# Kernel tuning notes

Hardware: AMD Instinct MI355X
Metric: run time of the kernel (lower is better)

## Reference

```python
import jax, jax.numpy as jnp
import numpy as np

BS, GS, E, KMAX = 128, 2000, 128, 4
CLIP = 10.0
NEG = -1e30


def _gru(x, hprev, Wih, Whh, bih, bhh):
    # torch.nn.GRUCell math
    gi = x @ Wih.T + bih
    gh = hprev @ Whh.T + bhh
    ir, iz, i_n = jnp.split(gi, 3, axis=-1)
    hr, hz, h_n = jnp.split(gh, 3, axis=-1)
    r = jax.nn.sigmoid(ir + hr)
    z = jax.nn.sigmoid(iz + hz)
    n = jnp.tanh(i_n + r * h_n)
    return (1.0 - z) * n + z * hprev


def setup_inputs() -> dict:
    key = jax.random.key(0)
    it = iter(jax.random.split(key, 40))
    s = 1.0 / float(np.sqrt(E))
    u = lambda shape: jax.random.uniform(next(it), shape, jnp.float32, -s, s)
    inp = {
        "h": jax.random.normal(next(it), (BS, GS, E), jnp.float32),
        "rec": jax.random.randint(next(it), (BS, GS), 0, GS, dtype=jnp.int32),
        "context2": jax.random.normal(next(it), (BS, 9), jnp.float32),
        "visited_time": jax.random.randint(next(it), (BS, GS), 0, GS, dtype=jnp.int32),
        "last_action": jax.random.randint(next(it), (BS, 1), 0, GS, dtype=jnp.int32),
        "fixed_action": jax.random.randint(next(it), (BS, KMAX), 0, GS, dtype=jnp.int32),
    }
    for n in ["W_K1", "W_K2", "W_K3", "W_K4", "W_Q1", "W_Q2", "W_Q3", "W_Q4", "W_init"]:
        inp[n] = u((E, E))
    for n in ["b_init", "V1", "V2", "init_query"]:
        inp[n] = u((E,))
    for r in ["rnn1", "rnn2"]:
        inp[r + "_Wih"] = u((3 * E, E))
        inp[r + "_Whh"] = u((3 * E, E))
        inp[r + "_bih"] = u((3 * E,))
        inp[r + "_bhh"] = u((3 * E,))
    return inp


def _forward(h, rec, visited_time, last_action, fixed_action,
             W_K1, W_K2, W_K3, W_K4, W_Q1, W_Q2, W_Q3, W_Q4, V1, V2,
             W_init, b_init, init_query,
             rnn1_Wih, rnn1_Whh, rnn1_bih, rnn1_bhh,
             rnn2_Wih, rnn2_Whh, rnn2_bih, rnn2_bhh):
    bs, gs, e = h.shape
    cols = jnp.arange(gs)[None, :]          # [1, gs]
    rows = jnp.arange(bs)
    # K projections of h are loop-invariant: hoist them (same math as in-loop recompute)
    K1h = jnp.einsum('bge,fe->bgf', h, W_K1)
    K2h = jnp.einsum('bge,fe->bgf', h, W_K2)
    K3h = jnp.einsum('bge,fe->bgf', h, W_K3)
    K4h = jnp.einsum('bge,fe->bgf', h, W_K4)
    q1 = q2 = h.mean(1) @ W_init.T + b_init
    input_q1 = input_q2 = jnp.broadcast_to(init_query, (bs, e))
    mask = jnp.zeros((bs, gs), bool)
    stopped = jnp.ones((bs,), bool)
    nol = jnp.full((bs, 1), -1, jnp.int32)   # next_of_last_action
    ai = jnp.zeros((bs, KMAX), jnp.int32)    # action_index
    kl = jnp.zeros((bs, KMAX + 1), jnp.int32)
    kr = jnp.zeros((bs, KMAX), jnp.int32)
    ll = jnp.zeros((bs,), h.dtype)
    vtt = None
    for i in range(KMAX):
        q1 = _gru(input_q1, q1, rnn1_Wih, rnn1_Whh, rnn1_bih, rnn1_bhh)
        q2 = _gru(input_q2, q2, rnn2_Wih, rnn2_Whh, rnn2_bih, rnn2_bhh)
        s1 = (V1 * jnp.tanh(K1h + (q1 @ W_Q1.T)[:, None, :] + K3h * (q1 @ W_Q3.T)[:, None, :])).sum(-1)
        s2 = (V2 * jnp.tanh(K2h + (q2 @ W_Q2.T)[:, None, :] + K4h * (q2 @ W_Q4.T)[:, None, :])).sum(-1)
        logits = jnp.tanh(s1 + s2) * CLIP
        logits = jnp.where(mask, NEG, logits)
        if i == 0:
            logits = jnp.where(cols == last_action, NEG, logits)
        action = fixed_action[:, i:i + 1]
        if i > 0:
            action = jnp.where(stopped[:, None], ai[:, 0:1], action)
        logp = jax.nn.log_softmax(logits, axis=-1)
        loss_now = jnp.take_along_axis(logp, action, 1)[:, 0]
        ll = ll + (loss_now if i == 0 else jnp.where(stopped, 0.0, loss_now))
        nna = jnp.take_along_axis(rec, action, 1)  # next_of_new_action [bs,1]
        ai = ai.at[:, i].set(action[:, 0])
        kl = kl.at[:, i].set(jnp.where(stopped, action[:, 0], kl[:, i]))
        kr = kr.at[:, (i - 1) % KMAX].set(jnp.where(stopped, kr[:, (i - 1) % KMAX], action[:, 0]))
        kl = kl.at[:, i + 1].set(nna[:, 0])
        input_q1 = h[rows, action[:, 0]]
        input_q2 = jnp.where(stopped[:, None], input_q1, h[rows, nol[:, 0] % gs])
        eq = (action == nol)[:, 0]
        stopped = eq if i == 0 else (stopped | eq)
        kl = kl.at[:, i].set(jnp.where(stopped, kl[:, (i - 1) % (KMAX + 1)], kl[:, i]))
        kr = kr.at[:, i].set(jnp.where(stopped, kr[:, (i - 1) % KMAX], kr[:, i]))
        if i == 0:
            vtt = (visited_time - jnp.take_along_axis(visited_time, action, 1)) % gs
        vtt_a = jnp.take_along_axis(vtt, action, 1)
        mask = vtt <= vtt_a
        if i == 0:
            mask = mask | (vtt > gs - 2)
        mask = jnp.where(stopped[:, None] & (cols == action), False, mask)
        allow = (~stopped) & (nna[:, 0] == ai[:, 0])
        mask = jnp.where(allow[:, None] & (cols == ai[:, 0:1]), False, mask)
        nol = jnp.where(stopped[:, None], jnp.int32(-1), nna)
    kr = kr.at[:, KMAX - 1].set(jnp.where(~stopped, kl[:, KMAX], kr[:, KMAX - 1]))
    action_all = jnp.concatenate([ai, kl[:, :KMAX], kr], axis=-1)  # [bs, 3*KMAX]
    return action_all, ll


def reference(h, rec, context2, visited_time, last_action, fixed_action,
              W_K1, W_K2, W_K3, W_K4, W_Q1, W_Q2, W_Q3, W_Q4,
              V1, V2, W_init, b_init, init_query,
              rnn1_Wih, rnn1_Whh, rnn1_bih, rnn1_bhh,
              rnn2_Wih, rnn2_Whh, rnn2_bih, rnn2_bhh):
    # context2 unused: with_explore_stat_feature=False path (learned V1/V2)
    return _forward(h, rec, visited_time, last_action, fixed_action,
                    W_K1, W_K2, W_K3, W_K4, W_Q1, W_Q2, W_Q3, W_Q4, V1, V2,
                    W_init, b_init, init_query,
                    rnn1_Wih, rnn1_Whh, rnn1_bih, rnn1_bhh,
                    rnn2_Wih, rnn2_Whh, rnn2_bih, rnn2_bhh)
```

## Files before the change

### kernel.cpp

```cpp
#include <hip/hip_runtime.h>
#include <math.h>

#define BS 128
#define GS 2000
#define E  128
#define KMAXI 4
#define CLIPV 10.0f
#define NEGV  -1.0e30f

typedef __bf16 bf16_t;
typedef __bf16 bf16x8 __attribute__((ext_vector_type(8)));
typedef float fx4 __attribute__((ext_vector_type(4)));
typedef float fx2 __attribute__((ext_vector_type(2)));

__device__ __forceinline__ float fast_sigmoid(float x){ return 1.0f/(1.0f+__expf(-x)); }
__device__ __forceinline__ float fast_tanhf(float x){
    float e = __expf(2.0f*x);
    return 1.0f - 2.0f/(e + 1.0f);
}
__device__ __forceinline__ float pade_tanh(float x){
    float t = __builtin_amdgcn_fmed3f(x, -3.0f, 3.0f);
    float r = t*t;
    float num = t*(27.0f + r);
    float den = fmaf(9.0f, r, 27.0f);
    return num * __builtin_amdgcn_rcpf(den);
}
__device__ __forceinline__ fx2 tanh2_poly(fx2 x){
    fx2 t;
    t.x = __builtin_amdgcn_fmed3f(x.x, -3.0f, 3.0f);
    t.y = __builtin_amdgcn_fmed3f(x.y, -3.0f, 3.0f);
    fx2 r = t*t;
    fx2 q = r*(-0.0015650f) + 0.03172875f;
    q = q*r + (-0.23082094f);
    q = q*r + 0.979947f;
    return t*q;
}
__device__ __forceinline__ int pymod_s(int a){ return a < 0 ? a + GS : a; }

__device__ __forceinline__ void load_lds16(const bf16_t* g, bf16_t* l){
    __builtin_amdgcn_global_load_lds(
        (const __attribute__((address_space(1))) void*)g,
        (__attribute__((address_space(3))) void*)l, 16, 0, 0);
}

#define SC_STRIDE 64

__global__ __launch_bounds__(256) void k_hmean(
    const float* __restrict__ h, float* __restrict__ hpart,
    const int* __restrict__ rec, const int* __restrict__ vtime,
    const int* __restrict__ last_action, const int* __restrict__ fixed_action,
    int* __restrict__ sc, float* __restrict__ out)
{
    int b = blockIdx.x, p = blockIdx.y, tid = threadIdx.x;
    if (p == 16){
        if (b != 0) return;
        int t = tid;
        if (t >= BS) return;
        int stopped = 1, nol = -1;
        int ai[4]={0,0,0,0}, kl[5]={0,0,0,0,0}, kr[4]={0,0,0,0};
        int a0 = 0;
        int* scb = sc + t*SC_STRIDE;
        for (int it=0; it<KMAXI; ++it){
            int action = (it==0) ? fixed_action[t*KMAXI]
                                 : (stopped ? ai[0] : fixed_action[t*KMAXI+it]);
            int old_stopped = stopped;
            if (it==0) a0 = action;
            int vta = (it==0) ? 0 : pymod_s(vtime[(size_t)t*GS+action] - vtime[(size_t)t*GS+a0]);
            int nna = rec[(size_t)t*GS+action];
            int eq  = (action == nol) ? 1 : 0;
            int new_stopped = (it==0) ? eq : (stopped | eq);
            int ai0 = (it==0) ? action : ai[0];
            int allow = (!new_stopped) && (nna == ai0);

            ai[it] = action;
            if (old_stopped)  kl[it] = action;
            if (!old_stopped) kr[(it+3)&3] = action;
            kl[it+1] = nna;
            if (new_stopped) kl[it] = kl[(it+4)%5];
            if (new_stopped) kr[it] = kr[(it+3)&3];

            int row1 = action;
            int i2 = pymod_s(nol);
            int row2 = old_stopped ? row1 : i2;

            int* s_it = scb + 8 + it*8;
            s_it[0]=action; s_it[1]=old_stopped; s_it[2]=new_stopped;
            s_it[3]=allow;  s_it[4]=vta; s_it[5]=row1; s_it[6]=row2;

            nol = new_stopped ? -1 : nna;
            stopped = new_stopped;
        }
        scb[0] = a0;
        if (!stopped) kr[3] = kl[4];
        out[BS*12 + t] = 0.0f;
        for (int j=0;j<4;++j) out[t*12+j]   = (float)ai[j];
        for (int j=0;j<4;++j) out[t*12+4+j] = (float)kl[j];
        for (int j=0;j<4;++j) out[t*12+8+j] = (float)kr[j];
        return;
    }
    int e4 = (tid & 31) * 4;
    int gsub = tid >> 5;
    float4 acc = {0.f,0.f,0.f,0.f};
    int g0 = p*125, g1 = g0+125;
    for (int g = g0 + gsub; g < g1; g += 8){
        float4 v = *(const float4*)(h + ((size_t)b*GS + g)*E + e4);
        acc.x += v.x; acc.y += v.y; acc.z += v.z; acc.w += v.w;
    }
    __shared__ float ps[8][E];
    *(float4*)(&ps[gsub][e4]) = acc;
    __syncthreads();
    if (tid < E){
        float s = 0.f;
        #pragma unroll
        for (int j=0;j<8;++j) s += ps[j][tid];
        hpart[(b*16+p)*E + tid] = s;
    }
}

__device__ __forceinline__ float dot32(const float* a, const float* __restrict__ w){
    const float4* a4=(const float4*)a; const float4* w4=(const float4*)w;
    float s=0.f;
    #pragma unroll 8
    for (int i=0;i<32;++i){ float4 x=a4[i], y=w4[i]; s += x.x*y.x + x.y*y.y + x.z*y.z + x.w*y.w; }
    return s;
}

__global__ __launch_bounds__(384) void k_gru4(
    const float* __restrict__ hpart, const float* __restrict__ W_init,
    const float* __restrict__ b_init, const float* __restrict__ init_query,
    const float* __restrict__ h, const int* __restrict__ sc,
    const float* __restrict__ Wih1, const float* __restrict__ Whh1,
    const float* __restrict__ bih1, const float* __restrict__ bhh1,
    const float* __restrict__ Wih2, const float* __restrict__ Whh2,
    const float* __restrict__ bih2, const float* __restrict__ bhh2,
    const float* __restrict__ WQ1, const float* __restrict__ WQ2,
    const float* __restrict__ WQ3, const float* __restrict__ WQ4,
    const float* __restrict__ WK1, const float* __restrict__ WK2,
    const float* __restrict__ WK3, const float* __restrict__ WK4,
    float* __restrict__ add_buf, bf16_t* __restrict__ Mb)
{
    int b = blockIdx.x, rnn = blockIdx.y, t = threadIdx.x;
    const float* Wih = rnn ? Wih2 : Wih1;
    const float* Whh = rnn ? Whh2 : Whh1;
    const float* bih = rnn ? bih2 : bih1;
    const float* bhh = rnn ? bhh2 : bhh1;
    const float* WQa = rnn ? WQ2 : WQ1;
    const float* WQm = rnn ? WQ4 : WQ3;
    const float* WKa = rnn ? WK2 : WK1;
    const float* WKm = rnn ? WK4 : WK3;

    __shared__ float xv[E], hv[E], mv[E];
    __shared__ float gi_s[3*E], gh_s[3*E];

    if (t < E){
        float s = 0.f;
        for (int p=0;p<16;++p) s += hpart[(b*16+p)*E + t];
        xv[t] = s * (1.0f/(float)GS);
    }
    __syncthreads();
    if (t < E) hv[t] = b_init[t] + dot32(xv, W_init + (size_t)t*E);
    __syncthreads();
    if (t < E) xv[t] = init_query[t];
    __syncthreads();

    for (int s=0; s<KMAXI; ++s){
        if (s>0){
            if (t < E){
                int row = sc[b*SC_STRIDE + 8 + (s-1)*8 + (rnn==0 ? 5 : 6)];
                xv[t] = h[((size_t)b*GS + row)*E + t];
            }
            __syncthreads();
        }
        {
            float gi = bih[t] + dot32(xv, Wih + (size_t)t*E);
            float gh = bhh[t] + dot32(hv, Whh + (size_t)t*E);
            gi_s[t] = gi; gh_s[t] = gh;
        }
        __syncthreads();
        if (t < E){
            float r = fast_sigmoid(gi_s[t]     + gh_s[t]);
            float z = fast_sigmoid(gi_s[t+E]   + gh_s[t+E]);
            float n = fast_tanhf  (gi_s[t+2*E] + r*gh_s[t+2*E]);
            hv[t] = (1.f-z)*n + z*hv[t];
        }
        __syncthreads();
        int slot = s*2 + rnn;
        if (t < 2*E){
            int r = t & (E-1);
            const float* W = (t < E) ? WQa : WQm;
            float v = dot32(hv, W + (size_t)r*E);
            if (t < E) add_buf[(size_t)slot*BS*E + b*E + r] = v;
            else       mv[r] = v;
        }
        __syncthreads();
        {
            bf16x8* outp = (bf16x8*)(Mb + ((size_t)slot*BS + b)*E*E);
            for (int u = t; u < 2048; u += 384){
                int f = u >> 4, e8 = u & 15;
                int e0 = e8*8;
                float mf = mv[f];
                float4 a0 = *(const float4*)(WKa + (size_t)f*E + e0);
                float4 a1 = *(const float4*)(WKa + (size_t)f*E + e0 + 4);
                float4 m0 = *(const float4*)(WKm + (size_t)f*E + e0);
                float4 m1 = *(const float4*)(WKm + (size_t)f*E + e0 + 4);
                bf16x8 o;
                o[0]=(bf16_t)(a0.x + m0.x*mf);
                o[1]=(bf16_t)(a0.y + m0.y*mf);
                o[2]=(bf16_t)(a0.z + m0.z*mf);
                o[3]=(bf16_t)(a0.w + m0.w*mf);
                o[4]=(bf16_t)(a1.x + m1.x*mf);
                o[5]=(bf16_t)(a1.y + m1.y*mf);
                o[6]=(bf16_t)(a1.z + m1.z*mf);
                o[7]=(bf16_t)(a1.w + m1.w*mf);
                outp[f*16 + (e8 ^ (f&7))] = o;
            }
        }
        __syncthreads();
    }
}

__global__ __launch_bounds__(256,2) void k_scores(
    const float* __restrict__ hf, const bf16_t* __restrict__ Mb,
    const float* __restrict__ add_buf,
    const float* __restrict__ V1, const float* __restrict__ V2,
    float* __restrict__ raw4)
{
    __shared__ bf16_t sM[2][E*E];
    int b = blockIdx.x, yc = blockIdx.y, tid = threadIdx.x;
    int wave = tid >> 6, lane = tid & 63;
    int qd = lane >> 4, cl = lane & 15;
    int gbase = yc*128 + wave*32;

    float vv_r[2][8];
    #pragma unroll
    for (int tf=0; tf<8; ++tf){
        vv_r[0][tf] = V1[tf*16+cl];
        vv_r[1][tf] = V2[tf*16+cl];
    }

    bf16x8 afr[2][4];
    #pragma unroll
    for (int set=0; set<2; ++set){
        int grow = gbase + set*16 + cl;
        if (grow >= GS) grow = GS-1;
        const float* hrow = hf + ((size_t)b*GS + grow)*E;
        #pragma unroll
        for (int s=0;s<4;++s){
            const float* p = hrow + s*32 + qd*8;
            float4 u0 = *(const float4*)(p);
            float4 u1 = *(const float4*)(p+4);
            bf16x8 a;
            a[0]=(bf16_t)u0.x; a[1]=(bf16_t)u0.y; a[2]=(bf16_t)u0.z; a[3]=(bf16_t)u0.w;
            a[4]=(bf16_t)u1.x; a[5]=(bf16_t)u1.y; a[6]=(bf16_t)u1.z; a[7]=(bf16_t)u1.w;
            afr[set][s]=a;
        }
    }

    for (int it=0; it<KMAXI; ++it){
        fx2 s00={0.f,0.f}, s01={0.f,0.f}, s10={0.f,0.f}, s11={0.f,0.f};

        const bf16_t* G0 = Mb + ((size_t)(it*2+0)*BS + b)*E*E;
        const bf16_t* G1 = Mb + ((size_t)(it*2+1)*BS + b)*E*E;
        float av_r[2][8];
        #pragma unroll
        for (int tf=0; tf<8; ++tf){
            av_r[0][tf] = add_buf[(size_t)(it*2+0)*BS*E + b*E + tf*16+cl];
            av_r[1][tf] = add_buf[(size_t)(it*2+1)*BS*E + b*E + tf*16+cl];
        }

        __syncthreads();
        #pragma unroll
        for (int j=0;j<8;++j){
            int c = wave*512 + j*64 + lane;
            load_lds16(G0 + (size_t)c*8, &sM[0][0] + (size_t)c*8);
            load_lds16(G1 + (size_t)c*8, &sM[1][0] + (size_t)c*8);
        }
        __syncthreads();

        #pragma unroll
        for (int arm=0; arm<2; ++arm){
            const bf16_t* sMc = &sM[arm][0];
            #pragma unroll
            for (int tf=0; tf<8; ++tf){
                int f = tf*16 + cl;
                bf16x8 b1[4];
                #pragma unroll
                for (int s=0;s<4;++s){
                    int e8 = s*4 + qd;
                    b1[s] = *(const bf16x8*)(sMc + ((size_t)(f*16 + (e8 ^ (f&7))))*8);
                }
                float av = av_r[arm][tf];
                fx4 a0 = {av,av,av,av};
                fx4 a1 = {av,av,av,av};
                #pragma unroll
                for (int s=0;s<4;++s){
                    a0 = __builtin_amdgcn_mfma_f32_16x16x32_bf16(afr[0][s], b1[s], a0, 0,0,0);
                    a1 = __builtin_amdgcn_mfma_f32_16x16x32_bf16(afr[1][s], b1[s], a1, 0,0,0);
                }
                fx2 vv2 = {vv_r[arm][tf], vv_r[arm][tf]};
                s00 += vv2 * tanh2_poly((fx2){a0[0], a0[1]});
                s01 += vv2 * tanh2_poly((fx2){a0[2], a0[3]});
                s10 += vv2 * tanh2_poly((fx2){a1[0], a1[1]});
                s11 += vv2 * tanh2_poly((fx2){a1[2], a1[3]});
            }
        }

        #pragma unroll
        for (int set=0;set<2;++set){
            fx2 pa = set ? s10 : s00;
            fx2 pb = set ? s11 : s01;
            float v[4] = {pa.x, pa.y, pb.x, pb.y};
            #pragma unroll
            for (int r=0;r<4;++r){
                float s = v[r];
                s += __shfl_xor(s, 1); s += __shfl_xor(s, 2);
                s += __shfl_xor(s, 4); s += __shfl_xor(s, 8);
                v[r] = s;
            }
            if (cl==0){
                int gi = gbase + set*16 + qd*4;
                if (gi+3 < GS){
                    float4 o;
                    o.x = CLIPV*pade_tanh(v[0]);
                    o.y = CLIPV*pade_tanh(v[1]);
                    o.z = CLIPV*pade_tanh(v[2]);
                    o.w = CLIPV*pade_tanh(v[3]);
                    *(float4*)(raw4 + ((size_t)it*BS + b)*GS + gi) = o;
                }
            }
        }
    }
}

__global__ __launch_bounds__(256) void k_ll(
    const float* __restrict__ raw4, const int* __restrict__ sc,
    const int* __restrict__ vtime, const int* __restrict__ last_action,
    float* __restrict__ out)
{
    __shared__ float sL[GS];
    __shared__ float red[256];
    int b = blockIdx.x, it = blockIdx.y, t = threadIdx.x;
    const int* scb = sc + b*SC_STRIDE;
    const int* s_it = scb + 8 + it*8;
    int action = s_it[0], olds = s_it[1];
    if (it>0 && olds) return;
    int a0 = scb[0];
    int la = last_action[b];
    int vt0 = vtime[(size_t)b*GS + a0];
    int ap=0, nsp=0, alp=0, vtp=0, p = it-1;
    if (it>0){
        const int* s_p = scb + 8 + p*8;
        ap = s_p[0]; nsp = s_p[2]; alp = s_p[3]; vtp = s_p[4];
    }
    for (int g=t; g<GS; g+=256){
        float l = raw4[((size_t)it*BS + b)*GS + g];
        int m;
        if (it==0){
            m = (g==la);
        } else {
            int d = vtime[(size_t)b*GS+g] - vt0;
            if (d < 0) d += GS;
            m = (d <= vtp) ? 1 : 0;
            if (p==0 && d > GS-2) m = 1;
            if (nsp && g==ap)     m = 0;
            if (alp && g==a0)     m = 0;
        }
        sL[g] = m ? NEGV : l;
    }
    __syncthreads();
    float mx = -3.0e38f;
    for (int g=t; g<GS; g+=256) mx = fmaxf(mx, sL[g]);
    red[t]=mx; __syncthreads();
    for (int s=128;s>0;s>>=1){ if(t<s) red[t]=fmaxf(red[t],red[t+s]); __syncthreads(); }
    mx = red[0]; __syncthreads();
    float sm = 0.f;
    for (int g=t; g<GS; g+=256) sm += __expf(sL[g]-mx);
    red[t]=sm; __syncthreads();
    for (int s=128;s>0;s>>=1){ if(t<s) red[t]+=red[t+s]; __syncthreads(); }
    if (t==0){
        float lse = mx + __logf(red[0]);
        atomicAdd(&out[BS*12 + b], sL[action] - lse);
    }
}

extern "C" void kernel_launch(void* const* d_in, const int* in_sizes, int n_in,
                              void* d_out, int out_size, void* d_ws, size_t ws_size,
                              hipStream_t stream)
{
    const float* h            = (const float*)d_in[0];
    const int*   rec          = (const int*)  d_in[1];
    const int*   vtime        = (const int*)  d_in[3];
    const int*   last_action  = (const int*)  d_in[4];
    const int*   fixed_action = (const int*)  d_in[5];
    const float* WK1=(const float*)d_in[6],  *WK2=(const float*)d_in[7];
    const float* WK3=(const float*)d_in[8],  *WK4=(const float*)d_in[9];
    const float* WQ1=(const float*)d_in[10], *WQ2=(const float*)d_in[11];
    const float* WQ3=(const float*)d_in[12], *WQ4=(const float*)d_in[13];
    const float* W_init=(const float*)d_in[14];
    const float* b_init=(const float*)d_in[15];
    const float* V1=(const float*)d_in[16], *V2=(const float*)d_in[17];
    const float* init_query=(const float*)d_in[18];
    const float* Wih1=(const float*)d_in[19], *Whh1=(const float*)d_in[20];
    const float* bih1=(const float*)d_in[21], *bhh1=(const float*)d_in[22];
    const float* Wih2=(const float*)d_in[23], *Whh2=(const float*)d_in[24];
    const float* bih2=(const float*)d_in[25], *bhh2=(const float*)d_in[26];
    float* out = (float*)d_out;

    char* ws = (char*)d_ws;
    size_t off = 0;
    auto alloc = [&](size_t bytes)->char*{
        char* p = ws + off; off += (bytes + 255) & ~(size_t)255; return p;
    };
    bf16_t* Mb     = (bf16_t*)alloc((size_t)8*BS*E*E*sizeof(bf16_t));
    float*  raw4   = (float*) alloc((size_t)KMAXI*BS*GS*sizeof(float));
    float*  add_buf= (float*) alloc((size_t)8*BS*E*sizeof(float));
    float*  hpart  = (float*) alloc((size_t)BS*16*E*sizeof(float));
    int*    sc     = (int*)   alloc((size_t)BS*SC_STRIDE*sizeof(int));
    (void)in_sizes; (void)n_in; (void)out_size; (void)ws_size;

    hipLaunchKernelGGL(k_hmean, dim3(BS,17), dim3(256), 0, stream,
                       h, hpart, rec, vtime, last_action, fixed_action, sc, out);
    hipLaunchKernelGGL(k_gru4, dim3(BS,2), dim3(384), 0, stream,
                       hpart, W_init, b_init, init_query, h, sc,
                       Wih1,Whh1,bih1,bhh1, Wih2,Whh2,bih2,bhh2,
                       WQ1,WQ2,WQ3,WQ4, WK1,WK2,WK3,WK4, add_buf, Mb);
    hipLaunchKernelGGL(k_scores, dim3(BS,16), dim3(256), 0, stream,
                       h, Mb, add_buf, V1, V2, raw4);
    hipLaunchKernelGGL(k_ll, dim3(BS, KMAXI), dim3(256), 0, stream,
                       raw4, sc, vtime, last_action, out);
}
```

Baseline: 431.2 us.

## Factor per-step key matrices into shared WK projections plus scalar add/mul terms

Instead of building a per-batch, per-step combined bf16 key matrix (WKa + m*WKm) in the GRU kernel and streaming it into the scores kernel, the scores kernel now computes h·WKa and h·WKm once with MFMA. It then applies the per-step add and multiply vectors elementwise for all four steps. This removes writing and reading roughly 8*BS*E*E bf16 of matrices and moves the WK bf16 conversion into a spare block of the first kernel. The cost is twice as many MFMAs per arm per tile, held once for all steps, plus more accumulator registers and a slightly different rounding order.

```diff
diff --git a/kernel.cpp b/kernel.cpp
--- a/kernel.cpp
+++ b/kernel.cpp
@@ -49,10 +49,27 @@
     const float* __restrict__ h, float* __restrict__ hpart,
     const int* __restrict__ rec, const int* __restrict__ vtime,
     const int* __restrict__ last_action, const int* __restrict__ fixed_action,
+    const float* __restrict__ WK1, const float* __restrict__ WK2,
+    const float* __restrict__ WK3, const float* __restrict__ WK4,
+    bf16_t* __restrict__ wkb,
     int* __restrict__ sc, float* __restrict__ out)
 {
     int b = blockIdx.x, p = blockIdx.y, tid = threadIdx.x;
     if (p == 16){
+        if (b >= 1 && b <= 4){
+            const float* W = (b==1)?WK1:(b==2)?WK2:(b==3)?WK3:WK4;
+            bf16x8* outp = (bf16x8*)(wkb + (size_t)(b-1)*E*E);
+            for (int u = tid; u < 2048; u += 256){
+                int f = u >> 4, e8 = u & 15;
+                float4 a0 = *(const float4*)(W + (size_t)f*E + e8*8);
+                float4 a1 = *(const float4*)(W + (size_t)f*E + e8*8 + 4);
+                bf16x8 o;
+                o[0]=(bf16_t)a0.x; o[1]=(bf16_t)a0.y; o[2]=(bf16_t)a0.z; o[3]=(bf16_t)a0.w;
+                o[4]=(bf16_t)a1.x; o[5]=(bf16_t)a1.y; o[6]=(bf16_t)a1.z; o[7]=(bf16_t)a1.w;
+                outp[f*16 + (e8 ^ (f&7))] = o;
+            }
+            return;
+        }
         if (b != 0) return;
         int t = tid;
         if (t >= BS) return;
@@ -135,9 +152,7 @@
     const float* __restrict__ bih2, const float* __restrict__ bhh2,
     const float* __restrict__ WQ1, const float* __restrict__ WQ2,
     const float* __restrict__ WQ3, const float* __restrict__ WQ4,
-    const float* __restrict__ WK1, const float* __restrict__ WK2,
-    const float* __restrict__ WK3, const float* __restrict__ WK4,
-    float* __restrict__ add_buf, bf16_t* __restrict__ Mb)
+    float* __restrict__ add_buf, float* __restrict__ mul_buf)
 {
     int b = blockIdx.x, rnn = blockIdx.y, t = threadIdx.x;
     const float* Wih = rnn ? Wih2 : Wih1;
@@ -146,10 +161,8 @@
     const float* bhh = rnn ? bhh2 : bhh1;
     const float* WQa = rnn ? WQ2 : WQ1;
     const float* WQm = rnn ? WQ4 : WQ3;
-    const float* WKa = rnn ? WK2 : WK1;
-    const float* WKm = rnn ? WK4 : WK3;
-
-    __shared__ float xv[E], hv[E], mv[E];
+
+    __shared__ float xv[E], hv[E];
     __shared__ float gi_s[3*E], gh_s[3*E];
 
     if (t < E){
@@ -184,52 +197,44 @@
             hv[t] = (1.f-z)*n + z*hv[t];
         }
         __syncthreads();
-        int slot = s*2 + rnn;
         if (t < 2*E){
             int r = t & (E-1);
             const float* W = (t < E) ? WQa : WQm;
             float v = dot32(hv, W + (size_t)r*E);
+            int slot = s*2 + rnn;
             if (t < E) add_buf[(size_t)slot*BS*E + b*E + r] = v;
-            else       mv[r] = v;
+            else       mul_buf[(size_t)slot*BS*E + b*E + r] = v;
         }
         __syncthreads();
-        {
-            bf16x8* outp = (bf16x8*)(Mb + ((size_t)slot*BS + b)*E*E);
-            for (int u = t; u < 2048; u += 384){
-                int f = u >> 4, e8 = u & 15;
-                int e0 = e8*8;
-                float mf = mv[f];
-                float4 a0 = *(const float4*)(WKa + (size_t)f*E + e0);
-                float4 a1 = *(const float4*)(WKa + (size_t)f*E + e0 + 4);
-                float4 m0 = *(const float4*)(WKm + (size_t)f*E + e0);
-                float4 m1 = *(const float4*)(WKm + (size_t)f*E + e0 + 4);
-                bf16x8 o;
-                o[0]=(bf16_t)(a0.x + m0.x*mf);
-                o[1]=(bf16_t)(a0.y + m0.y*mf);
-                o[2]=(bf16_t)(a0.z + m0.z*mf);
-                o[3]=(bf16_t)(a0.w + m0.w*mf);
-                o[4]=(bf16_t)(a1.x + m1.x*mf);
-                o[5]=(bf16_t)(a1.y + m1.y*mf);
-                o[6]=(bf16_t)(a1.z + m1.z*mf);
-                o[7]=(bf16_t)(a1.w + m1.w*mf);
-                outp[f*16 + (e8 ^ (f&7))] = o;
-            }
-        }
-        __syncthreads();
     }
 }
 
 __global__ __launch_bounds__(256,2) void k_scores(
-    const float* __restrict__ hf, const bf16_t* __restrict__ Mb,
-    const float* __restrict__ add_buf,
+    const float* __restrict__ hf, const bf16_t* __restrict__ wkb,
+    const float* __restrict__ add_buf, const float* __restrict__ mul_buf,
     const float* __restrict__ V1, const float* __restrict__ V2,
     float* __restrict__ raw4)
 {
-    __shared__ bf16_t sM[2][E*E];
+    __shared__ bf16_t sWa[E*E], sWm[E*E];
+    __shared__ float2 sMA[8*E];
     int b = blockIdx.x, yc = blockIdx.y, tid = threadIdx.x;
     int wave = tid >> 6, lane = tid & 63;
     int qd = lane >> 4, cl = lane & 15;
     int gbase = yc*128 + wave*32;
+
+    #pragma unroll
+    for (int j=0;j<8;++j){
+        int c = wave*512 + j*64 + lane;
+        load_lds16(wkb + 0*E*E + (size_t)c*8, sWa + (size_t)c*8);
+        load_lds16(wkb + 2*E*E + (size_t)c*8, sWm + (size_t)c*8);
+    }
+    for (int u = tid; u < 8*E; u += 256){
+        int slot = u >> 7, f = u & 127;
+        float2 ma;
+        ma.x = add_buf[(size_t)slot*BS*E + b*E + f];
+        ma.y = mul_buf[(size_t)slot*BS*E + b*E + f];
+        sMA[u] = ma;
+    }
 
     float vv_r[2][8];
     #pragma unroll
@@ -255,60 +260,73 @@
             afr[set][s]=a;
         }
     }
-
-    for (int it=0; it<KMAXI; ++it){
-        fx2 s00={0.f,0.f}, s01={0.f,0.f}, s10={0.f,0.f}, s11={0.f,0.f};
-
-        const bf16_t* G0 = Mb + ((size_t)(it*2+0)*BS + b)*E*E;
-        const bf16_t* G1 = Mb + ((size_t)(it*2+1)*BS + b)*E*E;
-        float av_r[2][8];
+    __syncthreads();
+
+    fx2 s_acc[4][4];
+    #pragma unroll
+    for (int it=0;it<4;++it)
+        #pragma unroll
+        for (int pr=0;pr<4;++pr) s_acc[it][pr] = (fx2){0.f,0.f};
+
+    #pragma unroll
+    for (int arm=0; arm<2; ++arm){
+        if (arm==1){
+            __syncthreads();
+            #pragma unroll
+            for (int j=0;j<8;++j){
+                int c = wave*512 + j*64 + lane;
+                load_lds16(wkb + 1*E*E + (size_t)c*8, sWa + (size_t)c*8);
+                load_lds16(wkb + 3*E*E + (size_t)c*8, sWm + (size_t)c*8);
+            }
+            __syncthreads();
+        }
         #pragma unroll
         for (int tf=0; tf<8; ++tf){
-            av_r[0][tf] = add_buf[(size_t)(it*2+0)*BS*E + b*E + tf*16+cl];
-            av_r[1][tf] = add_buf[(size_t)(it*2+1)*BS*E + b*E + tf*16+cl];
-        }
-
-        __syncthreads();
-        #pragma unroll
-        for (int j=0;j<8;++j){
-            int c = wave*512 + j*64 + lane;
-            load_lds16(G0 + (size_t)c*8, &sM[0][0] + (size_t)c*8);
-            load_lds16(G1 + (size_t)c*8, &sM[1][0] + (size_t)c*8);
-        }
-        __syncthreads();
-
-        #pragma unroll
-        for (int arm=0; arm<2; ++arm){
-            const bf16_t* sMc = &sM[arm][0];
-            #pragma unroll
-            for (int tf=0; tf<8; ++tf){
-                int f = tf*16 + cl;
-                bf16x8 b1[4];
-                #pragma unroll
-                for (int s=0;s<4;++s){
-                    int e8 = s*4 + qd;
-                    b1[s] = *(const bf16x8*)(sMc + ((size_t)(f*16 + (e8 ^ (f&7))))*8);
-                }
-                float av = av_r[arm][tf];
-                fx4 a0 = {av,av,av,av};
-                fx4 a1 = {av,av,av,av};
-                #pragma unroll
-                for (int s=0;s<4;++s){
-                    a0 = __builtin_amdgcn_mfma_f32_16x16x32_bf16(afr[0][s], b1[s], a0, 0,0,0);
-                    a1 = __builtin_amdgcn_mfma_f32_16x16x32_bf16(afr[1][s], b1[s], a1, 0,0,0);
-                }
-                fx2 vv2 = {vv_r[arm][tf], vv_r[arm][tf]};
-                s00 += vv2 * tanh2_poly((fx2){a0[0], a0[1]});
-                s01 += vv2 * tanh2_poly((fx2){a0[2], a0[3]});
-                s10 += vv2 * tanh2_poly((fx2){a1[0], a1[1]});
-                s11 += vv2 * tanh2_poly((fx2){a1[2], a1[3]});
-            }
-        }
-
+            int f = tf*16 + cl;
+            bf16x8 wa[4], wm[4];
+            #pragma unroll
+            for (int s=0;s<4;++s){
+                int e8 = s*4 + qd;
+                size_t idx = (size_t)(f*16 + (e8 ^ (f&7)))*8;
+                wa[s] = *(const bf16x8*)(sWa + idx);
+                wm[s] = *(const bf16x8*)(sWm + idx);
+            }
+            fx4 ta0 = {0.f,0.f,0.f,0.f}, ta1 = ta0, tm0 = ta0, tm1 = ta0;
+            #pragma unroll
+            for (int s=0;s<4;++s){
+                ta0 = __builtin_amdgcn_mfma_f32_16x16x32_bf16(afr[0][s], wa[s], ta0, 0,0,0);
+                ta1 = __builtin_amdgcn_mfma_f32_16x16x32_bf16(afr[1][s], wa[s], ta1, 0,0,0);
+                tm0 = __builtin_amdgcn_mfma_f32_16x16x32_bf16(afr[0][s], wm[s], tm0, 0,0,0);
+                tm1 = __builtin_amdgcn_mfma_f32_16x16x32_bf16(afr[1][s], wm[s], tm1, 0,0,0);
+            }
+            float2 ma[4];
+            #pragma unroll
+            for (int it=0;it<4;++it) ma[it] = sMA[(it*2+arm)*E + f];
+            float vvt = vv_r[arm][tf];
+            fx2 vv2 = {vvt, vvt};
+            #pragma unroll
+            for (int it=0;it<4;++it){
+                fx2 add2 = {ma[it].x, ma[it].x};
+                fx2 mul2 = {ma[it].y, ma[it].y};
+                fx2 x;
+                x = ((fx2){ta0[0],ta0[1]} + add2) + (fx2){tm0[0],tm0[1]}*mul2;
+                s_acc[it][0] += vv2 * tanh2_poly(x);
+                x = ((fx2){ta0[2],ta0[3]} + add2) + (fx2){tm0[2],tm0[3]}*mul2;
+                s_acc[it][1] += vv2 * tanh2_poly(x);
+                x = ((fx2){ta1[0],ta1[1]} + add2) + (fx2){tm1[0],tm1[1]}*mul2;
+                s_acc[it][2] += vv2 * tanh2_poly(x);
+                x = ((fx2){ta1[2],ta1[3]} + add2) + (fx2){tm1[2],tm1[3]}*mul2;
+                s_acc[it][3] += vv2 * tanh2_poly(x);
+            }
+        }
+    }
+
+    #pragma unroll
+    for (int it=0; it<4; ++it){
         #pragma unroll
         for (int set=0;set<2;++set){
-            fx2 pa = set ? s10 : s00;
-            fx2 pb = set ? s11 : s01;
+            fx2 pa = s_acc[it][set*2];
+            fx2 pb = s_acc[it][set*2+1];
             float v[4] = {pa.x, pa.y, pb.x, pb.y};
             #pragma unroll
             for (int r=0;r<4;++r){
@@ -411,21 +429,23 @@
     auto alloc = [&](size_t bytes)->char*{
         char* p = ws + off; off += (bytes + 255) & ~(size_t)255; return p;
     };
-    bf16_t* Mb     = (bf16_t*)alloc((size_t)8*BS*E*E*sizeof(bf16_t));
     float*  raw4   = (float*) alloc((size_t)KMAXI*BS*GS*sizeof(float));
     float*  add_buf= (float*) alloc((size_t)8*BS*E*sizeof(float));
+    float*  mul_buf= (float*) alloc((size_t)8*BS*E*sizeof(float));
     float*  hpart  = (float*) alloc((size_t)BS*16*E*sizeof(float));
     int*    sc     = (int*)   alloc((size_t)BS*SC_STRIDE*sizeof(int));
+    bf16_t* wkb    = (bf16_t*)alloc((size_t)4*E*E*sizeof(bf16_t));
     (void)in_sizes; (void)n_in; (void)out_size; (void)ws_size;
 
     hipLaunchKernelGGL(k_hmean, dim3(BS,17), dim3(256), 0, stream,
-                       h, hpart, rec, vtime, last_action, fixed_action, sc, out);
+                       h, hpart, rec, vtime, last_action, fixed_action,
+                       WK1, WK2, WK3, WK4, wkb, sc, out);
     hipLaunchKernelGGL(k_gru4, dim3(BS,2), dim3(384), 0, stream,
                        hpart, W_init, b_init, init_query, h, sc,
                        Wih1,Whh1,bih1,bhh1, Wih2,Whh2,bih2,bhh2,
-                       WQ1,WQ2,WQ3,WQ4, WK1,WK2,WK3,WK4, add_buf, Mb);
+                       WQ1,WQ2,WQ3,WQ4, add_buf, mul_buf);
     hipLaunchKernelGGL(k_scores, dim3(BS,16), dim3(256), 0, stream,
-                       h, Mb, add_buf, V1, V2, raw4);
+                       h, wkb, add_buf, mul_buf, V1, V2, raw4);
     hipLaunchKernelGGL(k_ll, dim3(BS, KMAXI), dim3(256), 0, stream,
                        raw4, sc, vtime, last_action, out);
 }
```

Result: slower. 1.121 ms (+160.0%).
